# Performance work log

Measured on AMD Instinct MI355X. Metric: run time of the kernel, lower is better.

The kernel has to match this reference:

```python
import jax, jax.numpy as jnp
import numpy as np

B, N, D, N_HOPS = 32, 1024, 128, 3
EPS = 1e-6


def setup_inputs() -> dict:
    key = jax.random.key(0)
    k1, k2, k3, k4 = jax.random.split(key, 4)
    # binary base adjacency (non-trainable buffer in the torch module)
    adj = (jax.random.uniform(k1, (N, N)) < 0.05).astype(jnp.float32)
    adj_weight = jax.random.uniform(k2, (B, N, N), dtype=jnp.float32)
    x = jax.random.normal(k3, (B, N, D), dtype=jnp.float32)
    W = jax.random.normal(k4, (D, D), dtype=jnp.float32) * 0.05
    b = jnp.zeros((D,), jnp.float32)
    a2 = jnp.ones((D,), jnp.float32)   # LayerNorm scale
    b2 = jnp.zeros((D,), jnp.float32)  # LayerNorm shift
    return {"x": x, "adj_weight": adj_weight, "adj": adj, "W": W, "b": b, "a2": a2, "b2": b2}


def _conv(x, adj_weight, adj):
    # adj_power squares the matrix each hop: hop h uses A^(2^h).
    # mask_h = (A^(2^h) == 1.0); weighted hop = (W^(2^h)) * mask_h.
    # propagate(edge_index from dense_to_sparse) == sum_j Wmask[b,j,i] * x[b,j]  (A^T x)
    A = adj            # [N, N]
    Wp = adj_weight    # [B, N, N]
    agg = jnp.zeros_like(x)
    for h in range(N_HOPS):
        mask = (A == 1.0).astype(x.dtype)          # [N, N]
        Wh = Wp * mask                              # [B, N, N]
        agg = agg + jnp.einsum('bji,bjd->bid', Wh, x)
        if h < N_HOPS - 1:
            A = A @ A
            Wp = jnp.matmul(Wp, Wp)
    return agg


def reference(x, adj_weight, adj, W, b, a2, b2):
    agg = _conv(x, adj_weight, adj)
    h = jnp.einsum('bnd,od->bno', agg, W) + b + x   # Linear + residual
    mean = jnp.mean(h, axis=-1, keepdims=True)
    std = jnp.std(h, axis=-1, keepdims=True, ddof=1)  # torch.std is unbiased
    y = a2 * (h - mean) / (std + EPS) + b2
    return y  # dropout p=0 (eval) -> identity
```

## Files before the change

### kernel.cpp

```cpp
#include <hip/hip_runtime.h>

#define NN 1024
#define BB 32
#define DD 128
#define EPSF 1e-6f
#define CAP 16384
#define NNNN ((size_t)NN * NN)

typedef __bf16 bf16x8 __attribute__((ext_vector_type(8)));
typedef float  f32x4  __attribute__((ext_vector_type(4)));
typedef unsigned short u16x8 __attribute__((ext_vector_type(8)));

typedef __attribute__((address_space(3))) unsigned int lds_u32;
typedef __attribute__((address_space(1))) const unsigned int glb_u32;

__device__ __forceinline__ lds_u32* lds_cast(const void* p) {
  return (lds_u32*)(unsigned int)(unsigned long long)p;
}
__device__ __forceinline__ glb_u32* glb_cast(const void* p) {
  return (glb_u32*)(unsigned long long)p;
}

__device__ __forceinline__ float bf2f(unsigned short u) {
  union { unsigned int i; float f; } v; v.i = ((unsigned int)u) << 16; return v.f;
}
__device__ __forceinline__ unsigned short f2bf(float f) {
  union { float f; unsigned int i; } v; v.f = f;
  unsigned int r = v.i + 0x7fffu + ((v.i >> 16) & 1u);
  return (unsigned short)(r >> 16);
}


__global__ __launch_bounds__(256) void convert_wp(const float* __restrict__ src,
    unsigned short* __restrict__ Wp, unsigned short* __restrict__ WpT) {
  __shared__ float tile[64][65];
  const int b = blockIdx.z;
  const int c0 = blockIdx.x * 64, r0 = blockIdx.y * 64;
  const int t = threadIdx.x;
  const int rr = t >> 3, cb = (t & 7) * 8;
  const size_t base = (size_t)b * NNNN;
#pragma unroll
  for (int p = 0; p < 2; ++p) {
    const int r = rr + p * 32;
    const float* srow = src + base + (size_t)(r0 + r) * NN + c0 + cb;
    f32x4 v0 = *(const f32x4*)srow;
    f32x4 v1 = *(const f32x4*)(srow + 4);
    u16x8 w;
#pragma unroll
    for (int j = 0; j < 4; ++j) { w[j] = f2bf(v0[j]); w[4 + j] = f2bf(v1[j]); }
    *(u16x8*)(Wp + base + (size_t)(r0 + r) * NN + c0 + cb) = w;
#pragma unroll
    for (int j = 0; j < 4; ++j) { tile[r][cb + j] = v0[j]; tile[r][cb + 4 + j] = v1[j]; }
  }
  __syncthreads();
#pragma unroll
  for (int p = 0; p < 2; ++p) {
    const int r = rr + p * 32;
    u16x8 w;
#pragma unroll
    for (int j = 0; j < 8; ++j) w[j] = f2bf(tile[cb + j][r]);
    *(u16x8*)(WpT + base + (size_t)(c0 + r) * NN + r0 + cb) = w;
  }
}

__global__ __launch_bounds__(256) void convert_x(const float* __restrict__ x,
    unsigned short* __restrict__ xT) {
  __shared__ float tile[32][33];
  const int b = blockIdx.z;
  const int d0 = blockIdx.x * 32, n0 = blockIdx.y * 32;
  const int tx = threadIdx.x, ty = threadIdx.y;
#pragma unroll
  for (int s = 0; s < 4; ++s) {
    int rr = ty + s * 8;
    tile[rr][tx] = x[(size_t)b * NN * DD + (size_t)(n0 + rr) * DD + d0 + tx];
  }
  __syncthreads();
#pragma unroll
  for (int s = 0; s < 4; ++s) {
    int rr = ty + s * 8;
    xT[(size_t)b * DD * NN + (size_t)(d0 + rr) * NN + n0 + tx] = f2bf(tile[tx][rr]);
  }
}

__global__ __launch_bounds__(256) void mask0cvt(const float* __restrict__ adj,
    unsigned char* __restrict__ mcode, unsigned short* __restrict__ adjbf,
    unsigned short* __restrict__ adjTbf) {
  __shared__ float tile[32][33];
  const int i0 = blockIdx.x * 32, j0 = blockIdx.y * 32;
  const int tx = threadIdx.x, ty = threadIdx.y;
#pragma unroll
  for (int s = 0; s < 4; ++s) {
    int rr = ty + s * 8;
    float v = adj[(size_t)(j0 + rr) * NN + i0 + tx];
    adjbf[(size_t)(j0 + rr) * NN + i0 + tx] = f2bf(v);
    tile[rr][tx] = v;
  }
  __syncthreads();
#pragma unroll
  for (int s = 0; s < 4; ++s) {
    int rr = ty + s * 8;
    float v = tile[tx][rr];
    adjTbf[(size_t)(i0 + rr) * NN + j0 + tx] = f2bf(v);
    mcode[(size_t)(i0 + rr) * NN + j0 + tx] = (v == 1.0f) ? 1 : 0;
  }
}

__global__ __launch_bounds__(256) void scan_a2(const float* __restrict__ P,
    unsigned short* __restrict__ A2, unsigned short* __restrict__ A2T,
    unsigned char* __restrict__ mcode) {
  __shared__ float tile[32][33];
  const int m0 = blockIdx.x * 32, n0 = blockIdx.y * 32;
  const int tx = threadIdx.x, ty = threadIdx.y;
#pragma unroll
  for (int s = 0; s < 4; ++s) {
    int rr = ty + s * 8;
    size_t idx = (size_t)(m0 + rr) * NN + n0 + tx;
    float v = P[idx] + P[NNNN + idx] + P[2 * NNNN + idx] + P[3 * NNNN + idx];
    A2[idx] = f2bf(v);
    tile[rr][tx] = v;
  }
  __syncthreads();
#pragma unroll
  for (int s = 0; s < 4; ++s) {
    int rr = ty + s * 8;
    float v = tile[tx][rr];
    A2T[(size_t)(n0 + rr) * NN + m0 + tx] = f2bf(v);
    if (v == 1.0f) mcode[(size_t)(n0 + rr) * NN + m0 + tx] |= 2;
  }
}

__global__ __launch_bounds__(256) void scan_a4(const float* __restrict__ P,
    unsigned int* __restrict__ entries, int* __restrict__ nnz) {
  size_t e = (size_t)blockIdx.x * 256 + threadIdx.x;
  float v = P[e] + P[NNNN + e] + P[2 * NNNN + e] + P[3 * NNNN + e];
  if (v == 1.0f) {
    int idx = atomicAdd(nnz, 1);
    if (idx < CAP) entries[idx] = ((unsigned)(e >> 10) << 16) | (unsigned)(e & 1023);
  }
}

#define BM 128
#define BN 128
#define BK 32

struct EpiWcomb {
  const unsigned char* mc;
  unsigned short* out;
  __device__ __forceinline__ void operator()(int b, int ks, int i, int j, float v) const {
    size_t idx = (size_t)i * NN + j;
    out[(size_t)b * NNNN + idx] = (mc[idx] & 2) ? f2bf(v) : (unsigned short)0;
  }
};

struct EpiSqPart {
  float* buf;
  __device__ __forceinline__ void operator()(int b, int ks, int i, int j, float v) const {
    buf[(size_t)ks * NNNN + (size_t)i * NN + j] = v;
  }
};

struct EpiAggPart {
  float* p0;
  float* p1;
  __device__ __forceinline__ void operator()(int b, int ks, int i, int d, float v) const {
    (ks ? p1 : p0)[(size_t)b * NN * DD + (size_t)i * DD + d] = v;
  }
};

#define LGKM_BARRIER() do { \
  asm volatile("s_waitcnt lgkmcnt(0)" ::: "memory"); \
  __builtin_amdgcn_s_barrier(); \
  asm volatile("" ::: "memory"); } while (0)

template <int MW, typename Epi>
__global__ __launch_bounds__(256, MW) void gemm_lds(
    const unsigned short* __restrict__ Ap, size_t sA,
    const unsigned short* __restrict__ Bp, size_t sB,
    int swz, int ksN, int nit, Epi epi) {
  __shared__ __align__(16) unsigned short As[3 * BM * BK];
  __shared__ __align__(16) unsigned short Bs[3 * BN * BK];
  int bx = blockIdx.x, by = blockIdx.y, z = blockIdx.z;
  if (swz == 1) {
    int lin = bx + (by << 3);
    int r = lin & 7, s = lin >> 3;
    bx = ((r & 3) << 1) | (s & 1);
    by = ((r >> 2) << 2) | (s >> 1);
  } else if (swz == 2) {
    int lin = bx + (by << 3) + (z << 6);
    int xcd = lin & 7, q = lin >> 3;
    z = xcd + ((q >> 6) << 3);
    int tile = q & 63;
    bx = tile & 7; by = tile >> 3;
  }
  const int b = z / ksN, ks = z - b * ksN;
  const int kbase = ks * nit * BK;
  const int tm = bx * BM, tn = by * BN;
  const unsigned short* Ab = Ap + (size_t)b * sA;
  const unsigned short* Bb = Bp + (size_t)b * sB;
  const int tid = threadIdx.x;
  const int w = tid >> 6, l = tid & 63;
  const int fr = l & 15, quad = l >> 4;
  const int moff = (w & 1) * 64, noff = (w >> 1) * 64;

  const int sr = l >> 2, ss = l & 3;
  const int r0 = w * 16 + sr;
  const int r1 = 64 + w * 16 + sr;
  const int kc0 = ss ^ ((r0 >> 1) & 3);
  const int kc1 = ss ^ ((r1 >> 1) & 3);
  const unsigned short* gA0 = Ab + (size_t)(tm + r0) * NN + kbase + kc0 * 8;
  const unsigned short* gA1 = Ab + (size_t)(tm + r1) * NN + kbase + kc1 * 8;
  const unsigned short* gB0 = Bb + (size_t)(tn + r0) * NN + kbase + kc0 * 8;
  const unsigned short* gB1 = Bb + (size_t)(tn + r1) * NN + kbase + kc1 * 8;

  f32x4 acc[4][4];
#pragma unroll
  for (int mi = 0; mi < 4; ++mi)
#pragma unroll
    for (int ni = 0; ni < 4; ++ni) acc[mi][ni] = (f32x4){0.f, 0.f, 0.f, 0.f};

  auto stage = [&](int off, int kt) {
    const size_t kk = (size_t)kt * BK;
    __builtin_amdgcn_global_load_lds(glb_cast(gA0 + kk),
        lds_cast(As + off + (w * 16) * BK), 16, 0, 0);
    __builtin_amdgcn_global_load_lds(glb_cast(gA1 + kk),
        lds_cast(As + off + (64 + w * 16) * BK), 16, 0, 0);
    __builtin_amdgcn_global_load_lds(glb_cast(gB0 + kk),
        lds_cast(Bs + off + (w * 16) * BK), 16, 0, 0);
    __builtin_amdgcn_global_load_lds(glb_cast(gB1 + kk),
        lds_cast(Bs + off + (64 + w * 16) * BK), 16, 0, 0);
  };
  auto compute = [&](const unsigned short* Ad, const unsigned short* Bd) {
    bf16x8 af[4], bfr[4];
#pragma unroll
    for (int mi = 0; mi < 4; ++mi) {
      int r = moff + mi * 16 + fr;
      int kc = quad ^ ((r >> 1) & 3);
      af[mi] = *(const bf16x8*)(Ad + r * BK + kc * 8);
    }
#pragma unroll
    for (int ni = 0; ni < 4; ++ni) {
      int r = noff + ni * 16 + fr;
      int kc = quad ^ ((r >> 1) & 3);
      bfr[ni] = *(const bf16x8*)(Bd + r * BK + kc * 8);
    }
#pragma unroll
    for (int mi = 0; mi < 4; ++mi)
#pragma unroll
      for (int ni = 0; ni < 4; ++ni)
        acc[mi][ni] = __builtin_amdgcn_mfma_f32_16x16x32_bf16(af[mi], bfr[ni], acc[mi][ni], 0, 0, 0);
  };

  stage(0, 0);
  stage(BM * BK, 1);
  int o0 = 0, o1 = BM * BK, o2 = 2 * BM * BK;
#pragma unroll 1
  for (int kt = 0; kt < nit; ++kt) {
    if (kt + 1 < nit) {
      asm volatile("s_waitcnt vmcnt(4)" ::: "memory");
    } else {
      asm volatile("s_waitcnt vmcnt(0)" ::: "memory");
    }
    __builtin_amdgcn_sched_barrier(0);
    __builtin_amdgcn_s_barrier();
    if (kt + 2 < nit) stage(o2, kt + 2);
    compute(As + o0, Bs + o0);
    int t = o0; o0 = o1; o1 = o2; o2 = t;
  }

#pragma unroll
  for (int mi = 0; mi < 4; ++mi)
#pragma unroll
    for (int ni = 0; ni < 4; ++ni)
#pragma unroll
      for (int t = 0; t < 4; ++t)
        epi(b, ks, tm + moff + mi * 16 + quad * 4 + t, tn + noff + ni * 16 + fr, acc[mi][ni][t]);
}

template <int MW, bool COMB, typename Epi>
__global__ __launch_bounds__(256, MW) void gemm_pipe(
    const unsigned short* __restrict__ Ap, size_t sA,
    const unsigned short* __restrict__ WtP, const unsigned char* __restrict__ McP,
    const unsigned short* __restrict__ Bp, size_t sB,
    int swz, int ksN, int nit, Epi epi) {
  __shared__ __align__(16) unsigned short As[2 * BM * BK];
  __shared__ __align__(16) unsigned short Bs[2 * BN * BK];
  int bx = blockIdx.x, by = blockIdx.y, z = blockIdx.z;
  if (swz == 1) {
    int lin = bx + (by << 3);
    int r = lin & 7, s = lin >> 3;
    bx = ((r & 3) << 1) | (s & 1);
    by = ((r >> 2) << 2) | (s >> 1);
  } else if (swz == 2) {
    int lin = bx + (z << 3);
    int xcd = lin & 7, q = lin >> 3;
    z = (xcd << 3) + (q >> 3);
    bx = q & 7;
  }
  const int b = z / ksN, ks = z - b * ksN;
  const int kbase = ks * nit * BK;
  const int tm = bx * BM, tn = by * BN;
  const unsigned short* Ab = Ap + (size_t)b * sA;
  const unsigned short* Bb = Bp + (size_t)b * sB;
  const unsigned short* Wb = COMB ? (WtP + (size_t)b * sA) : nullptr;
  const int tid = threadIdx.x;
  const int w = tid >> 6, l = tid & 63;
  const int lr = l >> 2, lc = l & 3;
  const int fr = l & 15, quad = l >> 4;
  const int moff = (w & 1) * 64, noff = (w >> 1) * 64;
  const int r0 = w * 16 + lr, r1 = (w + 4) * 16 + lr;
  const int kc0 = lc ^ ((r0 >> 1) & 3), kc1 = lc ^ ((r1 >> 1) & 3);
  const size_t ao0 = (size_t)(tm + r0) * NN + kbase + kc0 * 8;
  const size_t ao1 = (size_t)(tm + r1) * NN + kbase + kc1 * 8;
  const size_t bo0 = (size_t)(tn + r0) * NN + kbase + kc0 * 8;
  const size_t bo1 = (size_t)(tn + r1) * NN + kbase + kc1 * 8;
  const int ls0 = r0 * BK + lc * 8, ls1 = r1 * BK + lc * 8;

  unsigned short* const As0 = As;           unsigned short* const As1 = As + BM * BK;
  unsigned short* const Bs0 = Bs;           unsigned short* const Bs1 = Bs + BN * BK;

  f32x4 acc[4][4];
#pragma unroll
  for (int mi = 0; mi < 4; ++mi)
#pragma unroll
    for (int ni = 0; ni < 4; ++ni) acc[mi][ni] = (f32x4){0.f, 0.f, 0.f, 0.f};

  struct RegSet {
    u16x8 a0, a1, b0, b1;
    u16x8 w0, w1;
    unsigned long long m0, m1;
  };
  RegSet R0, R1;

  auto load = [&](RegSet& R, int kt) {
    size_t kk = (size_t)kt * BK;
    R.a0 = *(const u16x8*)(Ab + ao0 + kk);
    R.a1 = *(const u16x8*)(Ab + ao1 + kk);
    R.b0 = *(const u16x8*)(Bb + bo0 + kk);
    R.b1 = *(const u16x8*)(Bb + bo1 + kk);
    if constexpr (COMB) {
      R.w0 = *(const u16x8*)(Wb + ao0 + kk);
      R.w1 = *(const u16x8*)(Wb + ao1 + kk);
      R.m0 = *(const unsigned long long*)(McP + ao0 + kk);
      R.m1 = *(const unsigned long long*)(McP + ao1 + kk);
    }
  };
  auto wr = [&](const RegSet& R, unsigned short* Ad, unsigned short* Bd) {
    if constexpr (COMB) {
      u16x8 f0, f1;
#pragma unroll
      for (int j = 0; j < 8; ++j) {
        float s0 = bf2f(R.a0[j]);
        if ((R.m0 >> (8 * j)) & 1ull) s0 += bf2f(R.w0[j]);
        f0[j] = f2bf(s0);
        float s1 = bf2f(R.a1[j]);
        if ((R.m1 >> (8 * j)) & 1ull) s1 += bf2f(R.w1[j]);
        f1[j] = f2bf(s1);
      }
      *(u16x8*)(Ad + ls0) = f0;
      *(u16x8*)(Ad + ls1) = f1;
    } else {
      *(u16x8*)(Ad + ls0) = R.a0;
      *(u16x8*)(Ad + ls1) = R.a1;
    }
    *(u16x8*)(Bd + ls0) = R.b0;
    *(u16x8*)(Bd + ls1) = R.b1;
  };
  auto compute = [&](const unsigned short* Ad, const unsigned short* Bd) {
    bf16x8 af[4], bfr[4];
#pragma unroll
    for (int mi = 0; mi < 4; ++mi) {
      int r = moff + mi * 16 + fr;
      int kc = quad ^ ((r >> 1) & 3);
      af[mi] = *(const bf16x8*)(Ad + r * BK + kc * 8);
    }
#pragma unroll
    for (int ni = 0; ni < 4; ++ni) {
      int r = noff + ni * 16 + fr;
      int kc = quad ^ ((r >> 1) & 3);
      bfr[ni] = *(const bf16x8*)(Bd + r * BK + kc * 8);
    }
#pragma unroll
    for (int mi = 0; mi < 4; ++mi)
#pragma unroll
      for (int ni = 0; ni < 4; ++ni)
        acc[mi][ni] = __builtin_amdgcn_mfma_f32_16x16x32_bf16(af[mi], bfr[ni], acc[mi][ni], 0, 0, 0);
  };

  load(R0, 0);
  load(R1, 1);
  wr(R0, As0, Bs0);
  load(R0, 2);
  LGKM_BARRIER();
#pragma unroll 1
  for (int kt = 0; kt < nit - 2; kt += 2) {
    compute(As0, Bs0);
    wr(R1, As1, Bs1);
    if (kt + 3 < nit) load(R1, kt + 3);
    LGKM_BARRIER();
    compute(As1, Bs1);
    wr(R0, As0, Bs0);
    if (kt + 4 < nit) load(R0, kt + 4);
    LGKM_BARRIER();
  }
  compute(As0, Bs0);
  wr(R1, As1, Bs1);
  LGKM_BARRIER();
  compute(As1, Bs1);

#pragma unroll
  for (int mi = 0; mi < 4; ++mi)
#pragma unroll
    for (int ni = 0; ni < 4; ++ni)
#pragma unroll
      for (int t = 0; t < 4; ++t)
        epi(b, ks, tm + moff + mi * 16 + quad * 4 + t, tn + noff + ni * 16 + fr, acc[mi][ni][t]);
}

__global__ __launch_bounds__(256) void hop2_fix(const unsigned short* __restrict__ Wp,
    const unsigned short* __restrict__ WpT, const int* __restrict__ nnz,
    const unsigned int* __restrict__ entries, unsigned short* __restrict__ WcombT) {
  int n = *nnz;
  if (n > CAP) n = CAP;
  if (n == 0) return;
  __shared__ float rbuf[256];
  const int b = blockIdx.x;
  const size_t bnn = (size_t)b * NNNN;
  for (int e = blockIdx.y; e < n; e += gridDim.y) {
    unsigned int ent = entries[e];
    int j = ent >> 16, i = ent & 0xFFFF;
    float s = 0.f;
    for (int k = threadIdx.x; k < NN; k += 256) {
      float u = 0.f, v = 0.f;
      const unsigned short* wj  = Wp  + bnn + (size_t)j * NN;
      const unsigned short* wtk = WpT + bnn + (size_t)k * NN;
      const unsigned short* wk  = Wp  + bnn + (size_t)k * NN;
      const unsigned short* wti = WpT + bnn + (size_t)i * NN;
      for (int t = 0; t < NN; ++t) {
        u += bf2f(wj[t]) * bf2f(wtk[t]);
        v += bf2f(wk[t]) * bf2f(wti[t]);
      }
      s += u * v;
    }
    rbuf[threadIdx.x] = s;
    __syncthreads();
    for (int off = 128; off > 0; off >>= 1) {
      if (threadIdx.x < off) rbuf[threadIdx.x] += rbuf[threadIdx.x + off];
      __syncthreads();
    }
    if (threadIdx.x == 0) {
      size_t idx = bnn + (size_t)i * NN + j;
      WcombT[idx] = f2bf(bf2f(WcombT[idx]) + rbuf[0]);
    }
    __syncthreads();
  }
}

#define FROWS 16
__global__ __launch_bounds__(256) void fused_out(const float* __restrict__ a0p,
    const float* __restrict__ a1p, const float* __restrict__ x,
    const float* __restrict__ W, const float* __restrict__ bias,
    const float* __restrict__ g2, const float* __restrict__ bsh,
    float* __restrict__ out) {
  __shared__ unsigned short Wl[128 * 136];
  __shared__ float ar[256];
  __shared__ float wred[8];
  const int tid = threadIdx.x;
  for (int e = tid; e < 16384; e += 256) Wl[(e >> 7) * 136 + (e & 127)] = f2bf(W[e]);
  const int half = tid >> 7, o = tid & 127;
  const int w = tid >> 6, lane = tid & 63;
  const float bo = bias[o], go = g2[o], b2o = bsh[o];
  const size_t row0 = (size_t)blockIdx.x * FROWS;
  size_t rb = row0 * DD;
  float av = a0p[rb + tid] + a1p[rb + tid];
  float xv = x[rb + tid];
  __syncthreads();
  for (int rr = 0; rr < FROWS; rr += 2) {
    ar[tid] = av;
    const float xcur = xv;
    const size_t rbc = (row0 + rr) * DD;
    __syncthreads();
    if (rr + 2 < FROWS) {
      size_t rb2 = (row0 + rr + 2) * DD;
      av = a0p[rb2 + tid] + a1p[rb2 + tid];
      xv = x[rb2 + tid];
    }
    float hv = bo + xcur;
    const unsigned short* wrow = &Wl[o * 136];
    const float* arow = &ar[half * 128];
#pragma unroll
    for (int d8 = 0; d8 < 16; ++d8) {
      bf16x8 wv = *(const bf16x8*)(wrow + d8 * 8);
#pragma unroll
      for (int t = 0; t < 8; ++t) hv += (float)wv[t] * arow[d8 * 8 + t];
    }
    float s = hv, q = hv * hv;
#pragma unroll
    for (int off = 32; off > 0; off >>= 1) {
      s += __shfl_xor(s, off);
      q += __shfl_xor(q, off);
    }
    if (lane == 0) { wred[w] = s; wred[4 + w] = q; }
    __syncthreads();
    float st = wred[half * 2] + wred[half * 2 + 1];
    float qt = wred[4 + half * 2] + wred[4 + half * 2 + 1];
    float mean = st * (1.0f / 128.0f);
    float var = (qt - 128.0f * mean * mean) * (1.0f / 127.0f);
    var = fmaxf(var, 0.0f);
    float stdv = sqrtf(var);
    out[rbc + tid] = go * (hv - mean) / (stdv + EPSF) + b2o;
  }
}

extern "C" void kernel_launch(void* const* d_in, const int* in_sizes, int n_in,
                              void* d_out, int out_size, void* d_ws, size_t ws_size,
                              hipStream_t stream) {
  (void)in_sizes; (void)n_in; (void)out_size; (void)ws_size;
  const float* x    = (const float*)d_in[0];
  const float* adjw = (const float*)d_in[1];
  const float* adj  = (const float*)d_in[2];
  const float* W    = (const float*)d_in[3];
  const float* bias = (const float*)d_in[4];
  const float* a2   = (const float*)d_in[5];
  const float* b2   = (const float*)d_in[6];
  float* out = (float*)d_out;

  char* ws = (char*)d_ws;
  const size_t MB = 1048576;
  unsigned short* Wp_bf   = (unsigned short*)(ws);
  unsigned short* WpT_bf  = (unsigned short*)(ws + 64 * MB);
  unsigned short* WcombT  = (unsigned short*)(ws + 128 * MB);
  unsigned short* xT_bf   = (unsigned short*)(ws + 192 * MB);
  unsigned short* adj_bf  = (unsigned short*)(ws + 200 * MB);
  unsigned short* adjT_bf = (unsigned short*)(ws + 202 * MB);
  unsigned short* A2_bf   = (unsigned short*)(ws + 204 * MB);
  unsigned short* A2T_bf  = (unsigned short*)(ws + 206 * MB);
  float* sqpart           = (float*)(ws + 208 * MB);
  float* agg1             = (float*)(ws + 200 * MB);
  unsigned char* mcode    = (unsigned char*)(ws + 224 * MB);
  unsigned int* entries   = (unsigned int*)(ws + 225 * MB);
  int* nnz2               = (int*)(ws + 226 * MB);
  float* agg0 = out;

  hipMemsetAsync(nnz2, 0, 4, stream);

  dim3 blk32(32, 8, 1);
  convert_wp<<<dim3(16, 16, 32), 256, 0, stream>>>(adjw, Wp_bf, WpT_bf);
  convert_x<<<dim3(4, 32, 32), blk32, 0, stream>>>(x, xT_bf);
  mask0cvt<<<dim3(32, 32, 1), blk32, 0, stream>>>(adj, mcode, adj_bf, adjT_bf);

  gemm_lds<3><<<dim3(8, 8, 4), 256, 0, stream>>>(
      adj_bf, (size_t)0, adjT_bf, (size_t)0, 0, 4, 8, EpiSqPart{sqpart});
  scan_a2<<<dim3(32, 32, 1), blk32, 0, stream>>>(sqpart, A2_bf, A2T_bf, mcode);
  gemm_lds<3><<<dim3(8, 8, 4), 256, 0, stream>>>(
      A2_bf, (size_t)0, A2T_bf, (size_t)0, 0, 4, 8, EpiSqPart{sqpart});
  scan_a4<<<dim3(4096, 1, 1), 256, 0, stream>>>(sqpart, entries, nnz2);

  gemm_lds<3><<<dim3(8, 8, 32), 256, 0, stream>>>(
      WpT_bf, NNNN, Wp_bf, NNNN, 2, 1, NN / BK, EpiWcomb{mcode, WcombT});

  hop2_fix<<<dim3(32, 8, 1), 256, 0, stream>>>(Wp_bf, WpT_bf, nnz2, entries, WcombT);

  gemm_pipe<2, true><<<dim3(8, 1, 64), 256, 0, stream>>>(
      WcombT, NNNN, WpT_bf, mcode, xT_bf, (size_t)DD * NN, 2, 2, 16,
      EpiAggPart{agg0, agg1});

  fused_out<<<dim3(2048, 1, 1), 256, 0, stream>>>(agg0, agg1, x, W, bias, a2, b2, out);
}
```

Baseline: 477.6 us.

## Use 256x256-tile 8-wave GEMM with 4-stage pipeline for batched Wp squaring

Adds a new GEMM kernel with 256x256 output tiles, 512 threads (8 waves), and a 4-deep LDS ring of async global-to-LDS loads. It replaces the 128x128 gemm_lds in the dominant batched Wp·Wp product. Larger tiles raise arithmetic intensity and halve redundant global reads. The kernel also interleaves loads with MFMA and raises wave priority around the MFMA blocks. The cost is higher register pressure (32 accumulators per lane) and fewer blocks (512) to fill the CUs.

New measurement: 474.1 us. No clear change (-0.7%).

```diff
diff --git a/kernel.cpp b/kernel.cpp
--- a/kernel.cpp
+++ b/kernel.cpp
@@ -171,6 +171,125 @@
   asm volatile("s_waitcnt lgkmcnt(0)" ::: "memory"); \
   __builtin_amdgcn_s_barrier(); \
   asm volatile("" ::: "memory"); } while (0)
+
+#define TBM 256
+#define TBN 256
+#define TBK 32
+
+template <typename Epi>
+__global__ __launch_bounds__(512, 2) void gemm8(
+    const unsigned short* __restrict__ Ap, size_t sA,
+    const unsigned short* __restrict__ Bp, size_t sB,
+    int swz, int ksN, int nit, Epi epi) {
+  __shared__ __align__(16) unsigned short As[4 * TBM * TBK];
+  __shared__ __align__(16) unsigned short Bs[4 * TBN * TBK];
+  int bx = blockIdx.x, by = blockIdx.y, z = blockIdx.z;
+  if (swz == 2) {
+    int lin = bx + (by << 2) + (z << 4);
+    int xcd = lin & 7, rest = lin >> 3;
+    z = (xcd << 2) + (rest >> 4);
+    int tile = rest & 15;
+    bx = tile & 3; by = tile >> 2;
+  }
+  const int b = z / ksN, ks = z - b * ksN;
+  const int kbase = ks * nit * TBK;
+  const int tm = bx * TBM, tn = by * TBN;
+  const unsigned short* Ab = Ap + (size_t)b * sA;
+  const unsigned short* Bb = Bp + (size_t)b * sB;
+  const int tid = threadIdx.x;
+  const int w = tid >> 6, l = tid & 63;
+  const int fr = l & 15, quad = l >> 4;
+  const int wm = w >> 2, wn = w & 3;
+  const int kcq = (quad ^ ((fr >> 1) & 3)) * 8;
+
+  const int srow = l >> 2;
+  const int sgr = (l & 3) ^ ((l >> 3) & 3);
+  const unsigned short* gA0 = Ab + (size_t)(tm + w * 16 + srow) * NN + kbase + sgr * 8;
+  const unsigned short* gA1 = gA0 + (size_t)128 * NN;
+  const unsigned short* gB0 = Bb + (size_t)(tn + w * 16 + srow) * NN + kbase + sgr * 8;
+  const unsigned short* gB1 = gB0 + (size_t)128 * NN;
+
+  f32x4 acc[8][4];
+#pragma unroll
+  for (int mi = 0; mi < 8; ++mi)
+#pragma unroll
+    for (int ni = 0; ni < 4; ++ni) acc[mi][ni] = (f32x4){0.f, 0.f, 0.f, 0.f};
+
+  auto stageA = [&](int kt) {
+    unsigned short* base = As + (kt & 3) * (TBM * TBK);
+    const size_t kk = (size_t)kt * TBK;
+    __builtin_amdgcn_global_load_lds(glb_cast(gA0 + kk), lds_cast(base + (w * 16) * TBK), 16, 0, 0);
+    __builtin_amdgcn_global_load_lds(glb_cast(gA1 + kk), lds_cast(base + ((8 + w) * 16) * TBK), 16, 0, 0);
+  };
+  auto stageB = [&](int kt) {
+    unsigned short* base = Bs + (kt & 3) * (TBN * TBK);
+    const size_t kk = (size_t)kt * TBK;
+    __builtin_amdgcn_global_load_lds(glb_cast(gB0 + kk), lds_cast(base + (w * 16) * TBK), 16, 0, 0);
+    __builtin_amdgcn_global_load_lds(glb_cast(gB1 + kk), lds_cast(base + ((8 + w) * 16) * TBK), 16, 0, 0);
+  };
+
+  stageA(0); stageB(0);
+  stageA(1); stageB(1);
+  stageA(2); stageB(2);
+
+#pragma unroll 1
+  for (int kt = 0; kt < nit; ++kt) {
+    if (kt < nit - 2) {
+      asm volatile("s_waitcnt vmcnt(8)" ::: "memory");
+    } else if (kt == nit - 2) {
+      asm volatile("s_waitcnt vmcnt(4)" ::: "memory");
+    } else {
+      asm volatile("s_waitcnt vmcnt(0)" ::: "memory");
+    }
+    __builtin_amdgcn_sched_barrier(0);
+    __builtin_amdgcn_s_barrier();
+    __builtin_amdgcn_sched_barrier(0);
+
+    const unsigned short* Asl = As + (kt & 3) * (TBM * TBK);
+    const unsigned short* Bsl = Bs + (kt & 3) * (TBN * TBK);
+
+    if (kt + 3 < nit) stageA(kt + 3);
+    bf16x8 bf[4], af[4];
+#pragma unroll
+    for (int ni = 0; ni < 4; ++ni)
+      bf[ni] = *(const bf16x8*)(Bsl + (wn * 64 + ni * 16 + fr) * TBK + kcq);
+#pragma unroll
+    for (int mi = 0; mi < 4; ++mi)
+      af[mi] = *(const bf16x8*)(Asl + (wm * 128 + mi * 16 + fr) * TBK + kcq);
+    asm volatile("s_waitcnt lgkmcnt(0)" ::: "memory");
+    __builtin_amdgcn_sched_barrier(0);
+    __builtin_amdgcn_s_setprio(1);
+#pragma unroll
+    for (int mi = 0; mi < 4; ++mi)
+#pragma unroll
+      for (int ni = 0; ni < 4; ++ni)
+        acc[mi][ni] = __builtin_amdgcn_mfma_f32_16x16x32_bf16(af[mi], bf[ni], acc[mi][ni], 0, 0, 0);
+    __builtin_amdgcn_s_setprio(0);
+
+    if (kt + 3 < nit) stageB(kt + 3);
+#pragma unroll
+    for (int mi = 0; mi < 4; ++mi)
+      af[mi] = *(const bf16x8*)(Asl + (wm * 128 + (mi + 4) * 16 + fr) * TBK + kcq);
+    asm volatile("s_waitcnt lgkmcnt(0)" ::: "memory");
+    __builtin_amdgcn_sched_barrier(0);
+    __builtin_amdgcn_s_setprio(1);
+#pragma unroll
+    for (int mi = 0; mi < 4; ++mi)
+#pragma unroll
+      for (int ni = 0; ni < 4; ++ni)
+        acc[mi + 4][ni] = __builtin_amdgcn_mfma_f32_16x16x32_bf16(af[mi], bf[ni], acc[mi + 4][ni], 0, 0, 0);
+    __builtin_amdgcn_s_setprio(0);
+  }
+
+#pragma unroll
+  for (int mi = 0; mi < 8; ++mi)
+#pragma unroll
+    for (int ni = 0; ni < 4; ++ni)
+#pragma unroll
+      for (int t = 0; t < 4; ++t)
+        epi(b, ks, tm + wm * 128 + mi * 16 + quad * 4 + t,
+            tn + wn * 64 + ni * 16 + fr, acc[mi][ni][t]);
+}
 
 template <int MW, typename Epi>
 __global__ __launch_bounds__(256, MW) void gemm_lds(
@@ -185,12 +304,6 @@
     int r = lin & 7, s = lin >> 3;
     bx = ((r & 3) << 1) | (s & 1);
     by = ((r >> 2) << 2) | (s >> 1);
-  } else if (swz == 2) {
-    int lin = bx + (by << 3) + (z << 6);
-    int xcd = lin & 7, q = lin >> 3;
-    z = xcd + ((q >> 6) << 3);
-    int tile = q & 63;
-    bx = tile & 7; by = tile >> 3;
   }
   const int b = z / ksN, ks = z - b * ksN;
   const int kbase = ks * nit * BK;
@@ -555,8 +668,8 @@
       A2_bf, (size_t)0, A2T_bf, (size_t)0, 0, 4, 8, EpiSqPart{sqpart});
   scan_a4<<<dim3(4096, 1, 1), 256, 0, stream>>>(sqpart, entries, nnz2);
 
-  gemm_lds<3><<<dim3(8, 8, 32), 256, 0, stream>>>(
-      WpT_bf, NNNN, Wp_bf, NNNN, 2, 1, NN / BK, EpiWcomb{mcode, WcombT});
+  gemm8<<<dim3(4, 4, 32), 512, 0, stream>>>(
+      WpT_bf, NNNN, Wp_bf, NNNN, 2, 1, NN / TBK, EpiWcomb{mcode, WcombT});
 
   hop2_fix<<<dim3(32, 8, 1), 256, 0, stream>>>(Wp_bf, WpT_bf, nnz2, entries, WcombT);
 
```

## Use 256x256-tile 8-wave ping-pong GEMM for batched Wp squaring

Applied to the files above, without the earlier changes.

Replaces the 128x128 three-stage gemm_lds used for the batched Wp@Wp product with a new 512-thread kernel using 256x256 output tiles and BK=64. It double-buffers direct global-to-LDS loads, interleaves staging of A/B halves between four MFMA phases, raises wave priority around MFMA bursts, and maps batches to XCDs for L2 locality. The larger tile halves global traffic per FLOP, at the cost of high register pressure (128 accumulators per thread) and fewer blocks (512) per launch.

Measured after the change: 482.3 us. About the same (+1.0%).

```diff
diff --git a/kernel.cpp b/kernel.cpp
--- a/kernel.cpp
+++ b/kernel.cpp
@@ -171,6 +171,174 @@
   asm volatile("s_waitcnt lgkmcnt(0)" ::: "memory"); \
   __builtin_amdgcn_s_barrier(); \
   asm volatile("" ::: "memory"); } while (0)
+
+#define TBM 256
+#define TBN 256
+#define TBK 64
+#define AHALF (128 * TBK)
+#define ABUF  (TBM * TBK)
+
+template <typename Epi>
+__global__ __launch_bounds__(512, 2) void gemm8p(
+    const unsigned short* __restrict__ Ap,
+    const unsigned short* __restrict__ Bp,
+    int nt, Epi epi) {
+  __shared__ __align__(16) unsigned short As[2 * ABUF];
+  __shared__ __align__(16) unsigned short Bs[2 * ABUF];
+  const int lin = blockIdx.x + (blockIdx.y << 2) + (blockIdx.z << 4);
+  const int xcd = lin & 7, idx = lin >> 3;
+  const int b = xcd * 4 + (idx >> 4);
+  const int tile = idx & 15;
+  const int tm = (tile & 3) * TBM, tn = (tile >> 2) * TBN;
+  const unsigned short* Ab = Ap + (size_t)b * NNNN;
+  const unsigned short* Bb = Bp + (size_t)b * NNNN;
+  const int tid = threadIdx.x;
+  const int w = tid >> 6, l = tid & 63;
+  const int fr = l & 15, quad = l >> 4;
+  const int wm = w >> 2, wn = w & 3;
+
+  const int srow8 = l >> 3;
+  const int sgr = (l & 7) ^ srow8;
+  const unsigned short* gAh[2], * gBh[2];
+  gAh[0] = Ab + (size_t)(tm + w * 16 + srow8) * NN + sgr * 8;
+  gAh[1] = gAh[0] + (size_t)128 * NN;
+  gBh[0] = Bb + (size_t)(tn + w * 16 + srow8) * NN + sgr * 8;
+  gBh[1] = gBh[0] + (size_t)128 * NN;
+
+  auto stageA = [&](int t1, int h) {
+    unsigned short* dst = As + (t1 & 1) * ABUF + h * AHALF + (w * 16) * TBK;
+    const size_t kk = (size_t)t1 * TBK;
+    __builtin_amdgcn_global_load_lds(glb_cast(gAh[h] + kk), lds_cast(dst), 16, 0, 0);
+    __builtin_amdgcn_global_load_lds(glb_cast(gAh[h] + 8 * NN + kk), lds_cast(dst + 8 * TBK), 16, 0, 0);
+  };
+  auto stageB = [&](int t1, int h) {
+    unsigned short* dst = Bs + (t1 & 1) * ABUF + h * AHALF + (w * 16) * TBK;
+    const size_t kk = (size_t)t1 * TBK;
+    __builtin_amdgcn_global_load_lds(glb_cast(gBh[h] + kk), lds_cast(dst), 16, 0, 0);
+    __builtin_amdgcn_global_load_lds(glb_cast(gBh[h] + 8 * NN + kk), lds_cast(dst + 8 * TBK), 16, 0, 0);
+  };
+
+  const int grq0 = (((0 * 4 + quad) ^ (fr & 7))) * 8;
+  const int grq1 = (((1 * 4 + quad) ^ (fr & 7))) * 8;
+  const int brow = (wn & 1) * 64;
+
+  f32x4 acc[8][4];
+#pragma unroll
+  for (int mi = 0; mi < 8; ++mi)
+#pragma unroll
+    for (int ni = 0; ni < 4; ++ni) acc[mi][ni] = (f32x4){0.f, 0.f, 0.f, 0.f};
+
+  stageA(0, 0); stageA(0, 1);
+  stageB(0, 0); stageB(0, 1);
+
+#pragma unroll 1
+  for (int t = 0; t < nt; ++t) {
+    asm volatile("s_waitcnt vmcnt(0)" ::: "memory");
+    __builtin_amdgcn_sched_barrier(0);
+    __builtin_amdgcn_s_barrier();
+    __builtin_amdgcn_sched_barrier(0);
+    const unsigned short* Ad = As + (t & 1) * ABUF + wm * AHALF;
+    const unsigned short* Bd = Bs + (t & 1) * ABUF + (wn >> 1) * AHALF;
+    const int st = t + 1;
+    bf16x8 a0[4][2], a1[4][2], b0[2][2], b1[2][2];
+
+    if (st < nt) stageA(st, 0);
+#pragma unroll
+    for (int mi = 0; mi < 4; ++mi) {
+      const unsigned short* r = Ad + (mi * 16 + fr) * TBK;
+      a0[mi][0] = *(const bf16x8*)(r + grq0);
+      a0[mi][1] = *(const bf16x8*)(r + grq1);
+    }
+#pragma unroll
+    for (int ni = 0; ni < 2; ++ni) {
+      const unsigned short* r = Bd + (brow + ni * 16 + fr) * TBK;
+      b0[ni][0] = *(const bf16x8*)(r + grq0);
+      b0[ni][1] = *(const bf16x8*)(r + grq1);
+    }
+    __builtin_amdgcn_sched_barrier(0);
+    __builtin_amdgcn_s_barrier();
+    asm volatile("s_waitcnt lgkmcnt(0)" ::: "memory");
+    __builtin_amdgcn_sched_barrier(0);
+    __builtin_amdgcn_s_setprio(1);
+#pragma unroll
+    for (int mi = 0; mi < 4; ++mi)
+#pragma unroll
+      for (int ni = 0; ni < 2; ++ni) {
+        acc[mi][ni] = __builtin_amdgcn_mfma_f32_16x16x32_bf16(a0[mi][0], b0[ni][0], acc[mi][ni], 0, 0, 0);
+        acc[mi][ni] = __builtin_amdgcn_mfma_f32_16x16x32_bf16(a0[mi][1], b0[ni][1], acc[mi][ni], 0, 0, 0);
+      }
+    __builtin_amdgcn_s_setprio(0);
+    __builtin_amdgcn_s_barrier();
+
+    if (st < nt) stageB(st, 0);
+#pragma unroll
+    for (int ni = 0; ni < 2; ++ni) {
+      const unsigned short* r = Bd + (brow + (ni + 2) * 16 + fr) * TBK;
+      b1[ni][0] = *(const bf16x8*)(r + grq0);
+      b1[ni][1] = *(const bf16x8*)(r + grq1);
+    }
+    __builtin_amdgcn_sched_barrier(0);
+    __builtin_amdgcn_s_barrier();
+    asm volatile("s_waitcnt lgkmcnt(0)" ::: "memory");
+    __builtin_amdgcn_sched_barrier(0);
+    __builtin_amdgcn_s_setprio(1);
+#pragma unroll
+    for (int mi = 0; mi < 4; ++mi)
+#pragma unroll
+      for (int ni = 0; ni < 2; ++ni) {
+        acc[mi][ni + 2] = __builtin_amdgcn_mfma_f32_16x16x32_bf16(a0[mi][0], b1[ni][0], acc[mi][ni + 2], 0, 0, 0);
+        acc[mi][ni + 2] = __builtin_amdgcn_mfma_f32_16x16x32_bf16(a0[mi][1], b1[ni][1], acc[mi][ni + 2], 0, 0, 0);
+      }
+    __builtin_amdgcn_s_setprio(0);
+    __builtin_amdgcn_s_barrier();
+
+    if (st < nt) stageA(st, 1);
+#pragma unroll
+    for (int mi = 0; mi < 4; ++mi) {
+      const unsigned short* r = Ad + ((mi + 4) * 16 + fr) * TBK;
+      a1[mi][0] = *(const bf16x8*)(r + grq0);
+      a1[mi][1] = *(const bf16x8*)(r + grq1);
+    }
+    __builtin_amdgcn_sched_barrier(0);
+    __builtin_amdgcn_s_barrier();
+    asm volatile("s_waitcnt lgkmcnt(0)" ::: "memory");
+    __builtin_amdgcn_sched_barrier(0);
+    __builtin_amdgcn_s_setprio(1);
+#pragma unroll
+    for (int mi = 0; mi < 4; ++mi)
+#pragma unroll
+      for (int ni = 0; ni < 2; ++ni) {
+        acc[mi + 4][ni + 2] = __builtin_amdgcn_mfma_f32_16x16x32_bf16(a1[mi][0], b1[ni][0], acc[mi + 4][ni + 2], 0, 0, 0);
+        acc[mi + 4][ni + 2] = __builtin_amdgcn_mfma_f32_16x16x32_bf16(a1[mi][1], b1[ni][1], acc[mi + 4][ni + 2], 0, 0, 0);
+      }
+    __builtin_amdgcn_s_setprio(0);
+    __builtin_amdgcn_s_barrier();
+
+    if (st < nt) stageB(st, 1);
+    __builtin_amdgcn_sched_barrier(0);
+    __builtin_amdgcn_s_barrier();
+    __builtin_amdgcn_sched_barrier(0);
+    __builtin_amdgcn_s_setprio(1);
+#pragma unroll
+    for (int mi = 0; mi < 4; ++mi)
+#pragma unroll
+      for (int ni = 0; ni < 2; ++ni) {
+        acc[mi + 4][ni] = __builtin_amdgcn_mfma_f32_16x16x32_bf16(a1[mi][0], b0[ni][0], acc[mi + 4][ni], 0, 0, 0);
+        acc[mi + 4][ni] = __builtin_amdgcn_mfma_f32_16x16x32_bf16(a1[mi][1], b0[ni][1], acc[mi + 4][ni], 0, 0, 0);
+      }
+    __builtin_amdgcn_s_setprio(0);
+    __builtin_amdgcn_s_barrier();
+  }
+
+#pragma unroll
+  for (int mi = 0; mi < 8; ++mi)
+#pragma unroll
+    for (int ni = 0; ni < 4; ++ni)
+#pragma unroll
+      for (int tt = 0; tt < 4; ++tt)
+        epi(b, 0, tm + wm * 128 + mi * 16 + quad * 4 + tt,
+            tn + wn * 64 + ni * 16 + fr, acc[mi][ni][tt]);
+}
 
 template <int MW, typename Epi>
 __global__ __launch_bounds__(256, MW) void gemm_lds(
@@ -185,12 +353,6 @@
     int r = lin & 7, s = lin >> 3;
     bx = ((r & 3) << 1) | (s & 1);
     by = ((r >> 2) << 2) | (s >> 1);
-  } else if (swz == 2) {
-    int lin = bx + (by << 3) + (z << 6);
-    int xcd = lin & 7, q = lin >> 3;
-    z = xcd + ((q >> 6) << 3);
-    int tile = q & 63;
-    bx = tile & 7; by = tile >> 3;
   }
   const int b = z / ksN, ks = z - b * ksN;
   const int kbase = ks * nit * BK;
@@ -555,8 +717,8 @@
       A2_bf, (size_t)0, A2T_bf, (size_t)0, 0, 4, 8, EpiSqPart{sqpart});
   scan_a4<<<dim3(4096, 1, 1), 256, 0, stream>>>(sqpart, entries, nnz2);
 
-  gemm_lds<3><<<dim3(8, 8, 32), 256, 0, stream>>>(
-      WpT_bf, NNNN, Wp_bf, NNNN, 2, 1, NN / BK, EpiWcomb{mcode, WcombT});
+  gemm8p<<<dim3(4, 4, 32), 512, 0, stream>>>(
+      WpT_bf, Wp_bf, NN / TBK, EpiWcomb{mcode, WcombT});
 
   hop2_fix<<<dim3(32, 8, 1), 256, 0, stream>>>(Wp_bf, WpT_bf, nnz2, entries, WcombT);
 
```
